# Optimization experiments

Hardware: AMD Instinct MI355X
Metric: run time of the kernel (lower is better)

Reference implementation:

```python
import jax, jax.numpy as jnp
import numpy as np

T, N, F_IN, H1, H2, F_OUT = 48, 4096, 64, 64, 32, 64

def setup_inputs() -> dict:
    key = jax.random.key(0)
    ks = jax.random.split(key, 14)
    sc = 0.05
    x = jax.random.normal(ks[0], (T, N, F_IN), jnp.float32)
    adj = jax.random.uniform(ks[1], (N, N), jnp.float32) / N  # roughly row-normalized dense adjacency
    fc_w = jax.random.normal(ks[2], (F_IN, H1), jnp.float32) * sc
    fc_b = jnp.zeros((H1,), jnp.float32)
    Wz = jax.random.normal(ks[3], (H1, F_OUT), jnp.float32) * sc
    Wr = jax.random.normal(ks[4], (H1, F_OUT), jnp.float32) * sc
    Wh = jax.random.normal(ks[5], (H1, F_OUT), jnp.float32) * sc
    Lz = jax.random.normal(ks[6], (2 * F_OUT, F_OUT), jnp.float32) * sc
    Lr = jax.random.normal(ks[7], (2 * F_OUT, F_OUT), jnp.float32) * sc
    Lh = jax.random.normal(ks[8], (2 * F_OUT, F_OUT), jnp.float32) * sc
    bz = jnp.zeros((F_OUT,), jnp.float32)
    br = jnp.zeros((F_OUT,), jnp.float32)
    bh = jnp.zeros((F_OUT,), jnp.float32)
    return {"x": x, "adj": adj, "fc_w": fc_w, "fc_b": fc_b,
            "Wz": Wz, "Wr": Wr, "Wh": Wh,
            "Lz": Lz, "Lr": Lr, "Lh": Lh,
            "bz": bz, "br": br, "bh": bh}

def reference(x, adj, fc_w, fc_b, Wz, Wr, Wh, Lz, Lr, Lh, bz, br, bh):
    # relu(fc(x)) followed by relu(unsqueeze) == single relu
    xh = jax.nn.relu(x @ fc_w + fc_b)          # [T, N, H1]
    h0 = jnp.zeros((N, F_OUT), x.dtype)

    def step(h, xi):
        # TGCN cell: dense graph conv A @ (X W) feeding GRU-style gates
        az = adj @ (xi @ Wz)                   # [N, F_OUT]
        ar = adj @ (xi @ Wr)
        ah = adj @ (xi @ Wh)
        z = jax.nn.sigmoid(jnp.concatenate([az, h], axis=-1) @ Lz + bz)
        r = jax.nn.sigmoid(jnp.concatenate([ar, h], axis=-1) @ Lr + br)
        h_tilde = jnp.tanh(jnp.concatenate([ah, h * r], axis=-1) @ Lh + bh)
        h_new = z * h + (1.0 - z) * h_tilde
        return h_new, None

    h, _ = jax.lax.scan(step, h0, xh)
    return h[None]                              # [1, N, F_OUT]
```

## Files before the change

### kernel.cpp

```cpp
#include <hip/hip_runtime.h>

typedef unsigned short u16;
typedef unsigned char u8;
typedef short s16x8 __attribute__((ext_vector_type(8)));
typedef unsigned short u16x4 __attribute__((ext_vector_type(4)));
typedef float f32x4 __attribute__((ext_vector_type(4)));
typedef int i32x4 __attribute__((ext_vector_type(4)));
typedef int i32x8 __attribute__((ext_vector_type(8)));

#define AS1 __attribute__((address_space(1)))
#define AS3 __attribute__((address_space(3)))

__device__ __forceinline__ void g2l16(const void* g, void* l) {
  __builtin_amdgcn_global_load_lds((const AS1 void*)g, (AS3 void*)l, 16, 0, 0);
}

__device__ __forceinline__ float b2f(u16 u) {
  union { unsigned int i; float f; } x; x.i = ((unsigned int)u) << 16; return x.f;
}
__device__ __forceinline__ u16 f2b(float f) {
  unsigned int u = __builtin_bit_cast(unsigned int, f);
  return (u16)((u + 0x7fffu + ((u >> 16) & 1u)) >> 16);
}
__device__ __forceinline__ u8 f2e4m3(float v) {
  int p = __builtin_amdgcn_cvt_pk_fp8_f32(v, 0.f, 0, false);
  return (u8)(p & 0xff);
}
__device__ __forceinline__ float sigm(float x) { return 1.f / (1.f + __expf(-x)); }
__device__ __forceinline__ float tanh_f(float x) { return 2.f / (1.f + __expf(-2.f * x)) - 1.f; }


__global__ __launch_bounds__(256) void kpre(
    const float* __restrict__ a, u8* __restrict__ ab,
    const float* __restrict__ fcw, const float* __restrict__ fcb,
    const float* __restrict__ x, u8* __restrict__ xht,
    const float* __restrict__ Wz, const float* __restrict__ Wr, const float* __restrict__ Wh,
    const float* __restrict__ Lz, const float* __restrict__ Lr, const float* __restrict__ Lh,
    u16* __restrict__ wct, u16* __restrict__ lbt) {
  int b = blockIdx.x, tid = threadIdx.x;
  if (b < 4096) {
    size_t idx = (size_t)b * 256 + tid;
    const float4* src = (const float4*)a;
    unsigned int* dst = (unsigned int*)ab;
#pragma unroll
    for (int k = 0; k < 4; ++k) {
      float4 v = src[idx + (size_t)k * 1048576];
      unsigned int p = __builtin_amdgcn_cvt_pk_fp8_f32(v.x * 4096.f, v.y * 4096.f, 0, false);
      p = __builtin_amdgcn_cvt_pk_fp8_f32(v.z * 4096.f, v.w * 4096.f, p, true);
      dst[idx + (size_t)k * 1048576] = p;
    }
    return;
  }
  if (b < 4144) {
    int idx = (b - 4096) * 256 + tid;
    int c_cat = idx >> 6, hh = idx & 63;
    int g = c_cat >> 6, c = c_cat & 63;
    const float* W = (g == 0) ? Wz : (g == 1) ? Wr : Wh;
    const float* L = (g == 0) ? Lz : (g == 1) ? Lr : Lh;
    float acc = 0.f;
    for (int m = 0; m < 64; ++m) acc += W[hh * 64 + m] * L[m * 64 + c];
    wct[c_cat * 64 + hh] = f2b(acc);
    return;
  }
  if (b < 4147) {
    int g = b - 4144;
    const float* L = (g == 0) ? Lz : (g == 1) ? Lr : Lh;
    for (int i = 0; i < 16; ++i) {
      int idx = tid * 16 + i; int c = idx >> 6, hh = idx & 63;
      lbt[g * 4096 + c * 64 + hh] = f2b(L[(64 + hh) * 64 + c]);
    }
    return;
  }
  int kb = b - 4147;
  int t = kb >> 5, n0 = (kb & 31) * 128;
  __shared__ __align__(16) u16 xs[128 * 72];
  __shared__ __align__(16) u16 fw[64 * 72];
  __shared__ __align__(16) u8 xh8[64 * 128];
  __shared__ float fb[64];
  int w = tid >> 6, l = tid & 63;
#pragma unroll
  for (int i = 0; i < 16; ++i) {
    int idx = tid + i * 256;
    int h = idx & 63, f = idx >> 6;
    fw[h * 72 + f] = f2b(fcw[f * 64 + h]);
  }
  const float4* xg = (const float4*)(x + ((size_t)t * 4096 + n0) * 64);
#pragma unroll
  for (int i = 0; i < 8; ++i) {
    int f = tid + i * 256;
    float4 v = xg[f];
    u16x4 p; p[0] = f2b(v.x); p[1] = f2b(v.y); p[2] = f2b(v.z); p[3] = f2b(v.w);
    *(u16x4*)&xs[(f >> 4) * 72 + (f & 15) * 4] = p;
  }
  if (tid < 64) fb[tid] = fcb[tid];
  __syncthreads();

  int lm = l & 15, q = l >> 4;
  f32x4 acc[4][2];
#pragma unroll
  for (int i = 0; i < 4; ++i)
#pragma unroll
    for (int j = 0; j < 2; ++j)
#pragma unroll
      for (int r = 0; r < 4; ++r) acc[i][j][r] = 0.f;
#pragma unroll
  for (int s = 0; s < 2; ++s) {
    s16x8 af[4], bf[2];
#pragma unroll
    for (int i = 0; i < 4; ++i) af[i] = *(const s16x8*)&fw[(16 * i + lm) * 72 + 32 * s + q * 8];
#pragma unroll
    for (int j = 0; j < 2; ++j) bf[j] = *(const s16x8*)&xs[(32 * w + 16 * j + lm) * 72 + 32 * s + q * 8];
#pragma unroll
    for (int i = 0; i < 4; ++i)
#pragma unroll
      for (int j = 0; j < 2; ++j)
        acc[i][j] = __builtin_amdgcn_mfma_f32_16x16x32_bf16(af[i], bf[j], acc[i][j], 0, 0, 0);
  }
#pragma unroll
  for (int i = 0; i < 4; ++i)
#pragma unroll
    for (int j = 0; j < 2; ++j) {
      int node = 32 * w + 16 * j + lm;
      int h0 = 16 * i + q * 4;
#pragma unroll
      for (int r = 0; r < 4; ++r) {
        float v = acc[i][j][r] + fb[h0 + r];
        xh8[(h0 + r) * 128 + node] = f2e4m3(v > 0.f ? v : 0.f);
      }
    }
  __syncthreads();
  {
    int h = tid >> 2, seg = tid & 3;
    u8* dst = xht + (size_t)(t * 64 + h) * 4096 + n0 + seg * 32;
    const u8* src = &xh8[h * 128 + seg * 32];
    *(i32x4*)dst = *(const i32x4*)src;
    *(i32x4*)(dst + 16) = *(const i32x4*)(src + 16);
  }
}

__global__ __launch_bounds__(256) void k2(
    const u8* __restrict__ A, const u8* __restrict__ B, u16* __restrict__ M) {
  __shared__ __align__(16) u8 sh[40960];
  u8* As = sh;
  u8* Bs = sh + 16384;
  int tid = threadIdx.x, w = tid >> 6, l = tid & 63;
  int nt = blockIdx.x, mt = blockIdx.y;
  const u8* Ab = A + (size_t)mt * 128 * 4096;
  const u8* Bb = B + (size_t)nt * 192 * 4096;
  int lm = l & 15, q = l >> 4;
  int wm = w >> 1, wn = w & 1;
  f32x4 acc[4][6];
#pragma unroll
  for (int i = 0; i < 4; ++i)
#pragma unroll
    for (int j = 0; j < 6; ++j)
#pragma unroll
      for (int r = 0; r < 4; ++r) acc[i][j][r] = 0.f;
  int srow = l >> 3;
  for (int k0b = 0; k0b < 4096; k0b += 128) {
#pragma unroll
    for (int j = 0; j < 4; ++j) {
      int r0 = 32 * w + 8 * j;
      int row = r0 + srow;
      int c = ((l & 7) - row) & 7;
      g2l16(Ab + (size_t)row * 4096 + k0b + c * 16, (char*)As + r0 * 128);
    }
#pragma unroll
    for (int j = 0; j < 6; ++j) {
      int r0 = 48 * w + 8 * j;
      int row = r0 + srow;
      int c = ((l & 7) - row) & 7;
      g2l16(Bb + (size_t)row * 4096 + k0b + c * 16, (char*)Bs + r0 * 128);
    }
    __syncthreads();
    i32x8 a8[4];
#pragma unroll
    for (int i = 0; i < 4; ++i) {
      int ra = 64 * wm + 16 * i + lm;
      int p0 = (2 * q + ra) & 7, p1 = (2 * q + 1 + ra) & 7;
      i32x4 lo = *(const i32x4*)&As[ra * 128 + p0 * 16];
      i32x4 hi = *(const i32x4*)&As[ra * 128 + p1 * 16];
      a8[i] = __builtin_shufflevector(lo, hi, 0, 1, 2, 3, 4, 5, 6, 7);
    }
#pragma unroll
    for (int j = 0; j < 6; ++j) {
      int rb = 96 * wn + 16 * j + lm;
      int q0 = (2 * q + rb) & 7, q1 = (2 * q + 1 + rb) & 7;
      i32x4 lo2 = *(const i32x4*)&Bs[rb * 128 + q0 * 16];
      i32x4 hi2 = *(const i32x4*)&Bs[rb * 128 + q1 * 16];
      i32x8 b8 = __builtin_shufflevector(lo2, hi2, 0, 1, 2, 3, 4, 5, 6, 7);
#pragma unroll
      for (int i = 0; i < 4; ++i)
        acc[i][j] = __builtin_amdgcn_mfma_scale_f32_16x16x128_f8f6f4(
            a8[i], b8, acc[i][j], 0, 0, 0, 127, 0, 127);
    }
    __syncthreads();
  }
  u16* tb = (u16*)sh;
  const float sc = 1.f / 4096.f;
#pragma unroll
  for (int p = 0; p < 2; ++p) {
    if (p) __syncthreads();
    if (wm == p) {
#pragma unroll
      for (int i = 0; i < 4; ++i)
#pragma unroll
        for (int j = 0; j < 6; ++j)
#pragma unroll
          for (int r = 0; r < 4; ++r)
            tb[(16 * i + 4 * q + r) * 200 + 96 * wn + 16 * j + lm] = f2b(acc[i][j][r] * sc);
    }
    __syncthreads();
    int row = tid >> 2, seg = tid & 3;
    u16* dst = M + (size_t)(mt * 128 + p * 64 + row) * 3072 + nt * 192 + seg * 48;
    const u16* src = &tb[row * 200 + seg * 48];
#pragma unroll
    for (int v = 0; v < 6; ++v)
      *(i32x4*)(dst + 8 * v) = *(const i32x4*)(src + 8 * v);
  }
}

__global__ __launch_bounds__(256) void k3(
    const u16* __restrict__ M, const u16* __restrict__ wct, const u16* __restrict__ lbt,
    const float* __restrict__ bz, const float* __restrict__ br, const float* __restrict__ bh,
    float* __restrict__ out) {
  __shared__ __align__(16) u16 hhi[16 * 72], hlo[16 * 72];
  __shared__ __align__(16) u16 rhi[16 * 72], rlo[16 * 72];
  int tid = threadIdx.x, w = tid >> 6, l = tid & 63;
  int nb0 = blockIdx.x * 16;
  int lm = l & 15, q = l >> 4;
  int cb = 16 * w + q * 4;
  s16x8 afw[3][2], afl[3][2];
#pragma unroll
  for (int g = 0; g < 3; ++g)
#pragma unroll
    for (int s = 0; s < 2; ++s) {
      afw[g][s] = *(const s16x8*)&wct[(size_t)(g * 64 + 16 * w + lm) * 64 + 32 * s + q * 8];
      afl[g][s] = *(const s16x8*)&lbt[(size_t)(g * 64 + 16 * w + lm) * 64 + 32 * s + q * 8];
    }
  for (int i = tid; i < 16 * 72; i += 256) { hhi[i] = 0; hlo[i] = 0; }
  f32x4 bzv, brv, bhv, hv;
#pragma unroll
  for (int r = 0; r < 4; ++r) {
    bzv[r] = bz[cb + r]; brv[r] = br[cb + r]; bhv[r] = bh[cb + r]; hv[r] = 0.f;
  }
  __syncthreads();

  const u16* Mrow = M + (size_t)(nb0 + lm) * 3072;
  s16x8 Mn[2];
  Mn[0] = *(const s16x8*)&Mrow[q * 8];
  Mn[1] = *(const s16x8*)&Mrow[32 + q * 8];

  for (int t = 0; t < 48; ++t) {
    s16x8 Mc[2] = {Mn[0], Mn[1]};
    if (t < 47) {
      Mn[0] = *(const s16x8*)&Mrow[(t + 1) * 64 + q * 8];
      Mn[1] = *(const s16x8*)&Mrow[(t + 1) * 64 + 32 + q * 8];
    }
    f32x4 uzw, uzh, urw, urh;
#pragma unroll
    for (int r = 0; r < 4; ++r) { uzw[r] = 0.f; uzh[r] = 0.f; urw[r] = 0.f; urh[r] = 0.f; }
#pragma unroll
    for (int s = 0; s < 2; ++s) {
      s16x8 hh = *(const s16x8*)&hhi[lm * 72 + 32 * s + q * 8];
      s16x8 hl = *(const s16x8*)&hlo[lm * 72 + 32 * s + q * 8];
      uzw = __builtin_amdgcn_mfma_f32_16x16x32_bf16(afw[0][s], Mc[s], uzw, 0, 0, 0);
      uzh = __builtin_amdgcn_mfma_f32_16x16x32_bf16(afl[0][s], hh, uzh, 0, 0, 0);
      uzh = __builtin_amdgcn_mfma_f32_16x16x32_bf16(afl[0][s], hl, uzh, 0, 0, 0);
      urw = __builtin_amdgcn_mfma_f32_16x16x32_bf16(afw[1][s], Mc[s], urw, 0, 0, 0);
      urh = __builtin_amdgcn_mfma_f32_16x16x32_bf16(afl[1][s], hh, urh, 0, 0, 0);
      urh = __builtin_amdgcn_mfma_f32_16x16x32_bf16(afl[1][s], hl, urh, 0, 0, 0);
    }
    f32x4 zv, rv;
#pragma unroll
    for (int r = 0; r < 4; ++r) {
      zv[r] = sigm(uzw[r] + uzh[r] + bzv[r]);
      rv[r] = sigm(urw[r] + urh[r] + brv[r]);
    }
    {
      u16x4 phi, plo;
#pragma unroll
      for (int r = 0; r < 4; ++r) {
        float p = hv[r] * rv[r];
        u16 hi = f2b(p); phi[r] = hi; plo[r] = f2b(p - b2f(hi));
      }
      *(u16x4*)&rhi[lm * 72 + cb] = phi;
      *(u16x4*)&rlo[lm * 72 + cb] = plo;
    }
    __syncthreads();
    f32x4 uhw, uhh;
#pragma unroll
    for (int r = 0; r < 4; ++r) { uhw[r] = 0.f; uhh[r] = 0.f; }
#pragma unroll
    for (int s = 0; s < 2; ++s) {
      s16x8 rh = *(const s16x8*)&rhi[lm * 72 + 32 * s + q * 8];
      s16x8 rl = *(const s16x8*)&rlo[lm * 72 + 32 * s + q * 8];
      uhw = __builtin_amdgcn_mfma_f32_16x16x32_bf16(afw[2][s], Mc[s], uhw, 0, 0, 0);
      uhh = __builtin_amdgcn_mfma_f32_16x16x32_bf16(afl[2][s], rh, uhh, 0, 0, 0);
      uhh = __builtin_amdgcn_mfma_f32_16x16x32_bf16(afl[2][s], rl, uhh, 0, 0, 0);
    }
    {
      u16x4 phi, plo;
#pragma unroll
      for (int r = 0; r < 4; ++r) {
        float th = tanh_f(uhw[r] + uhh[r] + bhv[r]);
        float hn = zv[r] * hv[r] + (1.f - zv[r]) * th;
        hv[r] = hn;
        u16 hi = f2b(hn); phi[r] = hi; plo[r] = f2b(hn - b2f(hi));
      }
      *(u16x4*)&hhi[lm * 72 + cb] = phi;
      *(u16x4*)&hlo[lm * 72 + cb] = plo;
    }
    __syncthreads();
  }
#pragma unroll
  for (int r = 0; r < 4; ++r)
    out[(size_t)(nb0 + lm) * 64 + cb + r] = hv[r];
}

extern "C" void kernel_launch(void* const* d_in, const int* in_sizes, int n_in,
                              void* d_out, int out_size, void* d_ws, size_t ws_size,
                              hipStream_t stream) {
  const float* x   = (const float*)d_in[0];
  const float* adj = (const float*)d_in[1];
  const float* fcw = (const float*)d_in[2];
  const float* fcb = (const float*)d_in[3];
  const float* Wz  = (const float*)d_in[4];
  const float* Wr  = (const float*)d_in[5];
  const float* Wh  = (const float*)d_in[6];
  const float* Lz  = (const float*)d_in[7];
  const float* Lr  = (const float*)d_in[8];
  const float* Lh  = (const float*)d_in[9];
  const float* bz  = (const float*)d_in[10];
  const float* br  = (const float*)d_in[11];
  const float* bh  = (const float*)d_in[12];
  char* ws = (char*)d_ws;
  u8*  xht  = (u8*)(ws);
  u8*  adj8 = (u8*)(ws + (size_t)12582912);
  u16* Mm   = (u16*)(ws + (size_t)29360128);
  u16* wct  = (u16*)(ws + (size_t)54525952);
  u16* lbt  = (u16*)(ws + (size_t)54550528);
  float* outp = (float*)d_out;

  hipLaunchKernelGGL(kpre, dim3(5683), dim3(256), 0, stream,
                     adj, adj8, fcw, fcb, x, xht, Wz, Wr, Wh, Lz, Lr, Lh, wct, lbt);
  hipLaunchKernelGGL(k2, dim3(16, 32), dim3(256), 0, stream, adj8, xht, Mm);
  hipLaunchKernelGGL(k3, dim3(256), dim3(256), 0, stream, Mm, wct, lbt, bz, br, bh, outp);
}
```

Before: 261.0 us.

## Enlarge k2 tile to 256 rows, double-buffer B in LDS, read A directly

The k2 GEMM now runs 512-thread blocks covering 256 rows of the adjacency, which halves the grid and doubles reuse of each B tile. B tiles are double-buffered in LDS so the next K-slice prefetch overlaps the current MFMAs, cutting one barrier per iteration. A fragments are now loaded directly from global memory into registers instead of staging through LDS. The catch is uncoalesced 32-byte global reads for A, which depend on cache hits, plus higher register and LDS pressure per block.

```diff
diff --git a/kernel.cpp b/kernel.cpp
--- a/kernel.cpp
+++ b/kernel.cpp
@@ -138,17 +138,16 @@
   }
 }
 
-__global__ __launch_bounds__(256) void k2(
+__global__ __launch_bounds__(512, 2) void k2(
     const u8* __restrict__ A, const u8* __restrict__ B, u16* __restrict__ M) {
-  __shared__ __align__(16) u8 sh[40960];
-  u8* As = sh;
-  u8* Bs = sh + 16384;
+  __shared__ __align__(16) u8 sh[49152];
   int tid = threadIdx.x, w = tid >> 6, l = tid & 63;
   int nt = blockIdx.x, mt = blockIdx.y;
-  const u8* Ab = A + (size_t)mt * 128 * 4096;
+  const u8* Ab = A + (size_t)mt * 256 * 4096;
   const u8* Bb = B + (size_t)nt * 192 * 4096;
   int lm = l & 15, q = l >> 4;
   int wm = w >> 1, wn = w & 1;
+  int srow = l >> 3, scol = l & 7;
   f32x4 acc[4][6];
 #pragma unroll
   for (int i = 0; i < 4; ++i)
@@ -156,39 +155,39 @@
     for (int j = 0; j < 6; ++j)
 #pragma unroll
       for (int r = 0; r < 4; ++r) acc[i][j][r] = 0.f;
-  int srow = l >> 3;
-  for (int k0b = 0; k0b < 4096; k0b += 128) {
-#pragma unroll
-    for (int j = 0; j < 4; ++j) {
-      int r0 = 32 * w + 8 * j;
-      int row = r0 + srow;
-      int c = ((l & 7) - row) & 7;
-      g2l16(Ab + (size_t)row * 4096 + k0b + c * 16, (char*)As + r0 * 128);
-    }
-#pragma unroll
-    for (int j = 0; j < 6; ++j) {
-      int r0 = 48 * w + 8 * j;
-      int row = r0 + srow;
-      int c = ((l & 7) - row) & 7;
-      g2l16(Bb + (size_t)row * 4096 + k0b + c * 16, (char*)Bs + r0 * 128);
-    }
-    __syncthreads();
+
+#define STAGE_B(bsel, kk)                                                     \
+  do {                                                                        \
+    _Pragma("unroll") for (int j = 0; j < 3; ++j) {                           \
+      int r0 = 24 * w + 8 * j;                                                \
+      int row = r0 + srow;                                                    \
+      int c = (scol - row) & 7;                                               \
+      g2l16(Bb + (size_t)row * 4096 + (kk) + c * 16,                          \
+            sh + (bsel) * 24576 + r0 * 128);                                  \
+    }                                                                         \
+  } while (0)
+
+  STAGE_B(0, 0);
+  __syncthreads();
+
+  for (int it = 0; it < 32; ++it) {
+    int k0b = it * 128;
+    int cur = it & 1;
     i32x8 a8[4];
 #pragma unroll
     for (int i = 0; i < 4; ++i) {
       int ra = 64 * wm + 16 * i + lm;
-      int p0 = (2 * q + ra) & 7, p1 = (2 * q + 1 + ra) & 7;
-      i32x4 lo = *(const i32x4*)&As[ra * 128 + p0 * 16];
-      i32x4 hi = *(const i32x4*)&As[ra * 128 + p1 * 16];
-      a8[i] = __builtin_shufflevector(lo, hi, 0, 1, 2, 3, 4, 5, 6, 7);
-    }
+      a8[i] = *(const i32x8*)(Ab + (size_t)ra * 4096 + k0b + q * 32);
+    }
+    if (it < 31) STAGE_B(cur ^ 1, k0b + 128);
+    const u8* Bs = sh + cur * 24576;
 #pragma unroll
     for (int j = 0; j < 6; ++j) {
       int rb = 96 * wn + 16 * j + lm;
       int q0 = (2 * q + rb) & 7, q1 = (2 * q + 1 + rb) & 7;
-      i32x4 lo2 = *(const i32x4*)&Bs[rb * 128 + q0 * 16];
-      i32x4 hi2 = *(const i32x4*)&Bs[rb * 128 + q1 * 16];
-      i32x8 b8 = __builtin_shufflevector(lo2, hi2, 0, 1, 2, 3, 4, 5, 6, 7);
+      i32x4 lo = *(const i32x4*)&Bs[rb * 128 + q0 * 16];
+      i32x4 hi = *(const i32x4*)&Bs[rb * 128 + q1 * 16];
+      i32x8 b8 = __builtin_shufflevector(lo, hi, 0, 1, 2, 3, 4, 5, 6, 7);
 #pragma unroll
       for (int i = 0; i < 4; ++i)
         acc[i][j] = __builtin_amdgcn_mfma_scale_f32_16x16x128_f8f6f4(
@@ -196,10 +195,12 @@
     }
     __syncthreads();
   }
+#undef STAGE_B
+
   u16* tb = (u16*)sh;
   const float sc = 1.f / 4096.f;
 #pragma unroll
-  for (int p = 0; p < 2; ++p) {
+  for (int p = 0; p < 4; ++p) {
     if (p) __syncthreads();
     if (wm == p) {
 #pragma unroll
@@ -211,11 +212,11 @@
             tb[(16 * i + 4 * q + r) * 200 + 96 * wn + 16 * j + lm] = f2b(acc[i][j][r] * sc);
     }
     __syncthreads();
-    int row = tid >> 2, seg = tid & 3;
-    u16* dst = M + (size_t)(mt * 128 + p * 64 + row) * 3072 + nt * 192 + seg * 48;
-    const u16* src = &tb[row * 200 + seg * 48];
-#pragma unroll
-    for (int v = 0; v < 6; ++v)
+    int row = tid >> 3, seg = tid & 7;
+    u16* dst = M + (size_t)(mt * 256 + p * 64 + row) * 3072 + nt * 192 + seg * 24;
+    const u16* src = &tb[row * 200 + seg * 24];
+#pragma unroll
+    for (int v = 0; v < 3; ++v)
       *(i32x4*)(dst + 8 * v) = *(const i32x4*)(src + 8 * v);
   }
 }
@@ -344,6 +345,6 @@
 
   hipLaunchKernelGGL(kpre, dim3(5683), dim3(256), 0, stream,
                      adj, adj8, fcw, fcb, x, xht, Wz, Wr, Wh, Lz, Lr, Lh, wct, lbt);
-  hipLaunchKernelGGL(k2, dim3(16, 32), dim3(256), 0, stream, adj8, xht, Mm);
+  hipLaunchKernelGGL(k2, dim3(16, 16), dim3(512), 0, stream, adj8, xht, Mm);
   hipLaunchKernelGGL(k3, dim3(256), dim3(256), 0, stream, Mm, wct, lbt, bz, br, bh, outp);
 }
```

New measurement: 303.0 us. +16.1%, slower.
